# Performance work log

Hardware: AMD Instinct MI355X
Metric: run time of the kernel (lower is better)

Reference implementation:

```python
import jax, jax.numpy as jnp
import numpy as np

B, S, H, NH, NF = 128, 1024, 768, 8, 8
FUSED = 3 * H + NF  # 2312


def _lin(k, o, i):
    return jax.random.normal(k, (o, i), jnp.float32) * (1.0 / np.sqrt(i))


def setup_inputs() -> dict:
    key = jax.random.key(0)
    ks = jax.random.split(key, 20)
    last_hidden = jax.random.normal(ks[0], (B, S, H), jnp.float32)
    arousal_feats = jax.random.normal(ks[1], (B, NF), jnp.float32)
    sep1 = jax.random.randint(ks[2], (B,), 2, 800)
    sep2 = jnp.minimum(sep1 + jax.random.randint(ks[3], (B,), 2, 200), S - 1)
    return {
        "last_hidden": last_hidden,
        "arousal_feats": arousal_feats,
        "sep1": sep1,
        "sep2": sep2,
        "in_proj_w": _lin(ks[4], 3 * H, H),
        "in_proj_b": jnp.zeros((3 * H,), jnp.float32),
        "out_w": _lin(ks[5], H, H),
        "out_b": jnp.zeros((H,), jnp.float32),
        "ln_g": jnp.ones((NF,), jnp.float32),
        "ln_b": jnp.zeros((NF,), jnp.float32),
        "va_w1": _lin(ks[6], 512, FUSED),
        "va_b1": jnp.zeros((512,), jnp.float32),
        "va_w2": _lin(ks[7], 128, 512),
        "va_b2": jnp.zeros((128,), jnp.float32),
        "va_w3": _lin(ks[8], 2, 128),
        "va_b3": jnp.zeros((2,), jnp.float32),
        "pol_w": _lin(ks[9], 3, FUSED),
        "pol_b": jnp.zeros((3,), jnp.float32),
        "aro_w": _lin(ks[10], 3, FUSED),
        "aro_b": jnp.zeros((3,), jnp.float32),
    }


def reference(last_hidden, arousal_feats, sep1, sep2, in_proj_w, in_proj_b,
              out_w, out_b, ln_g, ln_b, va_w1, va_b1, va_w2, va_b2,
              va_w3, va_b3, pol_w, pol_b, aro_w, aro_b):
    b, s, h = last_hidden.shape
    nh, dh = NH, h // NH
    pos = jnp.arange(s)[None, :]  # [1,S]
    # ragged boundaries -> masks (honors s1>1 / s2>s1+1 fallbacks to CLS token)
    text_mask = jnp.where((sep1 > 1)[:, None], (pos >= 1) & (pos < sep1[:, None]), pos == 0)
    asp_mask = jnp.where((sep2 > sep1 + 1)[:, None], (pos > sep1[:, None]) & (pos < sep2[:, None]), pos == 0)
    amf = asp_mask.astype(last_hidden.dtype)
    asp_query = (last_hidden * amf[..., None]).sum(1) / amf.sum(1)[:, None]  # [B,H]
    # MultiheadAttention with a single query per sample, keys/values masked to text span
    wq, wk, wv = jnp.split(in_proj_w, 3, axis=0)
    bq, bk, bv = jnp.split(in_proj_b, 3)
    q = (asp_query @ wq.T + bq).reshape(b, nh, dh)
    k = (last_hidden @ wk.T + bk).reshape(b, s, nh, dh)
    v = (last_hidden @ wv.T + bv).reshape(b, s, nh, dh)
    scale = 1.0 / np.sqrt(dh)
    scores = jnp.einsum('bhd,bshd->bhs', q, k) * scale
    scores = jnp.where(text_mask[:, None, :], scores, -jnp.inf)
    attn = jax.nn.softmax(scores, axis=-1)
    ctx = jnp.einsum('bhs,bshd->bhd', attn, v).reshape(b, h)
    cross = ctx @ out_w.T + out_b  # [B,H]
    # ArousalFeatureNorm ~ LayerNorm over feature dim
    mu = arousal_feats.mean(-1, keepdims=True)
    var = arousal_feats.var(-1, keepdims=True)
    aro_n = (arousal_feats - mu) / jnp.sqrt(var + 1e-5) * ln_g + ln_b
    fused = jnp.concatenate([last_hidden[:, 0], cross, asp_query, aro_n], axis=-1)
    hdn = jax.nn.gelu(fused @ va_w1.T + va_b1, approximate=False)
    hdn = jax.nn.gelu(hdn @ va_w2.T + va_b2, approximate=False)
    va = hdn @ va_w3.T + va_b3
    pol = fused @ pol_w.T + pol_b
    aro = fused @ aro_w.T + aro_b
    return (va, pol, aro)
```

## Files before the change

kernel.cpp:

```cpp
#include <hip/hip_runtime.h>
#include <hip/hip_bf16.h>
#include <math.h>

#define B 128
#define S 1024
#define H 768
#define NH 8
#define DH 96
#define FUSED 2312
#define KCHUNK 128
#define NOUT 544
#define MD 800
#define NZ_NOCTX 13
#define NZ_CTX 5
#define NZTOT 18
#define ASL 8
#define NSL 8
#define FCH 16
#define SCALE 0.10206207261596575f
#define GELU_C 0.70710678118654752f

#define MTILES (17 * 25)
#define HTILES (NZ_NOCTX * 4 * 17)

__device__ __forceinline__ float dot4(float4 a, float4 b) {
    return a.x * b.x + a.y * b.y + a.z * b.z + a.w * b.w;
}
__device__ __forceinline__ float gelu(float x) {
    return 0.5f * x * (1.0f + erff(x * GELU_C));
}

__device__ __forceinline__ const float* wrow_sel(int n, const float* va_w1,
                                                 const float* pol_w,
                                                 const float* aro_w,
                                                 bool& valid) {
    valid = true;
    if (n < 512) return va_w1 + (size_t)n * FUSED;
    if (n < 515) return pol_w + (size_t)(n - 512) * FUSED;
    if (n < 518) return aro_w + (size_t)(n - 515) * FUSED;
    valid = false;
    return va_w1;
}

__global__ __launch_bounds__(256) void k1_aspq_m(
        const float* __restrict__ lh,
        const int* __restrict__ sep1,
        const int* __restrict__ sep2,
        const float* __restrict__ va_w1,
        const float* __restrict__ pol_w,
        const float* __restrict__ aro_w,
        const float* __restrict__ out_w,
        const float* __restrict__ out_b,
        float* __restrict__ aspp,
        float* __restrict__ Mbuf) {
    int bid = blockIdx.x, t = threadIdx.x;
    if (bid < B * ASL) {
        if (t >= 192) return;
        int b = bid >> 3, z = bid & 7;
        int s1 = sep1[b], s2 = sep2[b];
        int lo, hi;
        if (s2 > s1 + 1) { lo = s1 + 1; hi = s2; } else { lo = 0; hi = 1; }
        const float* base = lh + ((size_t)b * S) * H + 4 * t;
        float4 a = {0.f, 0.f, 0.f, 0.f};
        for (int s = lo + z; s < hi; s += ASL) {
            float4 r = *(const float4*)(base + (size_t)s * H);
            a.x += r.x; a.y += r.y; a.z += r.z; a.w += r.w;
        }
        *(float4*)(aspp + (size_t)z * (B * H) + b * H + 4 * t) = a;
        return;
    }
    int j = bid - B * ASL;
    int n0 = (j / 25) * 32, d0 = (j % 25) * 32;
    __shared__ float As[32][33];
    __shared__ float Ws[32][33];
    int tx = t & 31, ty = t >> 5;
    int lr = t >> 3, lc = (t & 7) * 4;
    float acc[4] = {0.f, 0.f, 0.f, 0.f};
    for (int k0 = 0; k0 < H; k0 += 32) {
        {
            int n = n0 + lr;
            bool valid;
            const float* wr = wrow_sel(n, va_w1, pol_w, aro_w, valid);
            float4 a = {0.f, 0.f, 0.f, 0.f};
            if (valid) a = *(const float4*)(wr + H + k0 + lc);
            As[lr][lc] = a.x; As[lr][lc + 1] = a.y;
            As[lr][lc + 2] = a.z; As[lr][lc + 3] = a.w;
        }
        {
            int c = k0 + lr;
            float4 w;
            if (d0 < H) {
                w = *(const float4*)(out_w + (size_t)c * H + d0 + lc);
            } else {
                w.x = (lc == 0) ? out_b[c] : 0.f;
                w.y = 0.f; w.z = 0.f; w.w = 0.f;
            }
            Ws[lc][lr] = w.x; Ws[lc + 1][lr] = w.y;
            Ws[lc + 2][lr] = w.z; Ws[lc + 3][lr] = w.w;
        }
        __syncthreads();
#pragma unroll
        for (int kk = 0; kk < 32; ++kk) {
            float wv = Ws[tx][kk];
#pragma unroll
            for (int i = 0; i < 4; ++i)
                acc[i] += As[ty + 8 * i][kk] * wv;
        }
        __syncthreads();
    }
#pragma unroll
    for (int i = 0; i < 4; ++i)
        Mbuf[(size_t)(n0 + ty + 8 * i) * MD + d0 + tx] = acc[i];
}

__global__ void qu_kernel(const float* __restrict__ aspp,
                          const int* __restrict__ sep1,
                          const int* __restrict__ sep2,
                          const float* __restrict__ wq,
                          const float* __restrict__ bq,
                          const float* __restrict__ wk,
                          float* __restrict__ aspq,
                          float* __restrict__ U) {
    int b = blockIdx.x, h = blockIdx.y, t = threadIdx.x;
    int s1 = sep1[b], s2 = sep2[b];
    int lo, hi;
    if (s2 > s1 + 1) { lo = s1 + 1; hi = s2; } else { lo = 0; hi = 1; }
    float inv = 1.0f / (float)(hi - lo);
    __shared__ float aq[H];
    __shared__ float qh[DH];
    for (int c = t; c < H; c += 256) {
        float a = 0.f;
#pragma unroll
        for (int z = 0; z < ASL; ++z)
            a += aspp[(size_t)z * (B * H) + b * H + c];
        a *= inv;
        aq[c] = a;
        if (h == 0) aspq[b * H + c] = a;
    }
    __syncthreads();
    int wave = t >> 6, lane = t & 63;
#pragma unroll
    for (int i = 0; i < 24; ++i) {
        int d = wave * 24 + i;
        const float* wrow = wq + (size_t)(h * DH + d) * H;
        float a = 0.f;
#pragma unroll
        for (int j = 0; j < H / 64; ++j) a += wrow[lane + 64 * j] * aq[lane + 64 * j];
        for (int off = 32; off; off >>= 1) a += __shfl_xor(a, off);
        if (lane == 0) qh[d] = a + bq[h * DH + d];
    }
    __syncthreads();
    float u0 = 0.f, u1 = 0.f, u2 = 0.f;
    for (int d = 0; d < DH; ++d) {
        const float* wrow = wk + (size_t)(h * DH + d) * H;
        float qd = qh[d];
        u0 += qd * wrow[t];
        u1 += qd * wrow[t + 256];
        u2 += qd * wrow[t + 512];
    }
    float* Ub = U + ((size_t)b * NH + h) * H;
    Ub[t] = u0; Ub[t + 256] = u1; Ub[t + 512] = u2;
}

__global__ __launch_bounds__(512) void k3_flash_hdn1(
        const float* __restrict__ lhg,
        const float* __restrict__ U,
        const int* __restrict__ sep1,
        const float* __restrict__ aspq,
        const float* __restrict__ aro_f,
        const float* __restrict__ ln_g,
        const float* __restrict__ ln_b,
        const float* __restrict__ va_w1,
        const float* __restrict__ pol_w,
        const float* __restrict__ aro_w,
        float* __restrict__ Op,
        float* __restrict__ mlb,
        float* __restrict__ hdn1p) {
    __shared__ float smem[FCH * H];
    int bid = blockIdx.x, t = threadIdx.x;

    if (bid < B * NSL) {
        int b = bid >> 3, z = bid & 7;
        int wave = t >> 6, lane = t & 63;
        int s1 = sep1[b];
        int tlo = (s1 > 1) ? 1 : 0;
        int thi = (s1 > 1) ? s1 : 1;
        int span = thi - tlo;
        int nrows = (span > z) ? ((span - z - 1) / NSL + 1) : 0;
        float (*lhs)[H] = (float(*)[H])smem;

        const float4* Uh = (const float4*)(U + ((size_t)b * NH + wave) * H);
        float4 u0 = Uh[lane], u1 = Uh[lane + 64], u2 = Uh[lane + 128];
        float4 O0 = {0.f, 0.f, 0.f, 0.f}, O1 = O0, O2 = O0;
        float m = -1e30f, l = 0.f;
        int rid = t >> 5, cid = t & 31;

        for (int j0 = 0; j0 < nrows; j0 += FCH) {
            int nv = min(FCH, nrows - j0);
            if (rid < nv) {
                int sg = tlo + z + NSL * (j0 + rid);
                const float4* row = (const float4*)(lhg + ((size_t)b * S + sg) * H);
                float4* dst = (float4*)lhs[rid];
#pragma unroll
                for (int k = 0; k < 6; ++k) dst[cid + 32 * k] = row[cid + 32 * k];
            }
            __syncthreads();
            for (int r = 0; r < nv; ++r) {
                const float4* xr = (const float4*)lhs[r];
                float4 x0 = xr[lane], x1 = xr[lane + 64], x2 = xr[lane + 128];
                float s = dot4(u0, x0) + dot4(u1, x1) + dot4(u2, x2);
                for (int off = 32; off; off >>= 1) s += __shfl_xor(s, off);
                s *= SCALE;
                if (s <= m) {
                    float p = __expf(s - m);
                    l += p;
                    O0.x += p * x0.x; O0.y += p * x0.y; O0.z += p * x0.z; O0.w += p * x0.w;
                    O1.x += p * x1.x; O1.y += p * x1.y; O1.z += p * x1.z; O1.w += p * x1.w;
                    O2.x += p * x2.x; O2.y += p * x2.y; O2.z += p * x2.z; O2.w += p * x2.w;
                } else {
                    float c = __expf(m - s);
                    m = s;
                    l = l * c + 1.0f;
                    O0.x = O0.x * c + x0.x; O0.y = O0.y * c + x0.y;
                    O0.z = O0.z * c + x0.z; O0.w = O0.w * c + x0.w;
                    O1.x = O1.x * c + x1.x; O1.y = O1.y * c + x1.y;
                    O1.z = O1.z * c + x1.z; O1.w = O1.w * c + x1.w;
                    O2.x = O2.x * c + x2.x; O2.y = O2.y * c + x2.y;
                    O2.z = O2.z * c + x2.z; O2.w = O2.w * c + x2.w;
                }
            }
            __syncthreads();
        }
        float4* Ob = (float4*)(Op + (((size_t)z * B + b) * NH + wave) * H);
        Ob[lane] = O0; Ob[lane + 64] = O1; Ob[lane + 128] = O2;
        if (lane == 0) {
            float* ml = mlb + ((size_t)z * B + b) * NH * 2;
            ml[2 * wave]     = m;
            ml[2 * wave + 1] = l;
        }
        return;
    }

    int j = bid - B * NSL;
    int z13 = j / 68, rem = j % 68;
    int z = (z13 < 6) ? z13 : z13 + 6;
    int m0 = (rem / 17) * 32, n0 = (rem % 17) * 32;
    int kbase = z * KCHUNK;
    float (*As)[33] = (float(*)[33])smem;
    float (*Ws)[33] = (float(*)[33])(smem + 32 * 33);
    int tx = t & 31, ty = t >> 5;
    int lr = t >> 3, lc = (t & 7) * 4;
    float acc[4] = {0.f, 0.f, 0.f, 0.f};
    bool active = (t < 256);
    for (int k0 = kbase; k0 < kbase + KCHUNK; k0 += 32) {
        if (active) {
            int bb = m0 + lr;
            int k = k0 + lc;
            float4 a;
            if (k < 768) {
                a = *(const float4*)(lhg + (size_t)bb * S * H + k);
            } else if (k < 2304) {
                a = *(const float4*)(aspq + (size_t)bb * H + (k - 1536));
            } else if (k < FUSED) {
                const float* af = aro_f + bb * 8;
                float mu = 0.f;
#pragma unroll
                for (int jj = 0; jj < 8; ++jj) mu += af[jj];
                mu *= 0.125f;
                float var = 0.f;
#pragma unroll
                for (int jj = 0; jj < 8; ++jj) { float d = af[jj] - mu; var += d * d; }
                var *= 0.125f;
                float rs = rsqrtf(var + 1e-5f);
                int c = k - 2304;
                a.x = (af[c]     - mu) * rs * ln_g[c]     + ln_b[c];
                a.y = (af[c + 1] - mu) * rs * ln_g[c + 1] + ln_b[c + 1];
                a.z = (af[c + 2] - mu) * rs * ln_g[c + 2] + ln_b[c + 2];
                a.w = (af[c + 3] - mu) * rs * ln_g[c + 3] + ln_b[c + 3];
            } else {
                a = {0.f, 0.f, 0.f, 0.f};
            }
            As[lr][lc] = a.x; As[lr][lc + 1] = a.y;
            As[lr][lc + 2] = a.z; As[lr][lc + 3] = a.w;
            int n = n0 + lr;
            int kk = min(k0 + lc, FUSED - 4);
            bool valid;
            const float* wr = wrow_sel(n, va_w1, pol_w, aro_w, valid);
            float4 w = {0.f, 0.f, 0.f, 0.f};
            if (valid) w = *(const float4*)(wr + kk);
            Ws[lr][lc] = w.x; Ws[lr][lc + 1] = w.y;
            Ws[lr][lc + 2] = w.z; Ws[lr][lc + 3] = w.w;
        }
        __syncthreads();
        if (active) {
#pragma unroll
            for (int kk = 0; kk < 32; ++kk) {
                float wv = Ws[tx][kk];
#pragma unroll
                for (int i = 0; i < 4; ++i)
                    acc[i] += As[ty + 8 * i][kk] * wv;
            }
        }
        __syncthreads();
    }
    if (active) {
        int n = n0 + tx;
#pragma unroll
        for (int i = 0; i < 4; ++i) {
            int mm = m0 + ty + 8 * i;
            hdn1p[(size_t)z13 * (B * NOUT) + (size_t)mm * NOUT + n] = acc[i];
        }
    }
}

__global__ void mergectx_kernel(const float* __restrict__ Op,
                                const float* __restrict__ mlb,
                                const float* __restrict__ wv,
                                const float* __restrict__ bv,
                                float* __restrict__ ctx) {
    int b = blockIdx.x, h = blockIdx.y, t = threadIdx.x;
    float M = -1e30f;
#pragma unroll
    for (int z = 0; z < NSL; ++z)
        M = fmaxf(M, mlb[(((size_t)z * B + b) * NH + h) * 2]);
    float wz[NSL], L = 0.f;
#pragma unroll
    for (int z = 0; z < NSL; ++z) {
        const float* ml = mlb + (((size_t)z * B + b) * NH + h) * 2;
        float e = __expf(ml[0] - M);
        wz[z] = e;
        L += e * ml[1];
    }
    float Li = 1.0f / L;
    __shared__ float wsum[H];
    for (int c = t; c < H; c += 256) {
        float a = 0.f;
#pragma unroll
        for (int z = 0; z < NSL; ++z)
            a += wz[z] * Op[(((size_t)z * B + b) * NH + h) * H + c];
        wsum[c] = a * Li;
    }
    __syncthreads();
    int wave = t >> 6, lane = t & 63;
#pragma unroll
    for (int i = 0; i < 24; ++i) {
        int d = wave * 24 + i;
        const float* wrow = wv + (size_t)(h * DH + d) * H;
        float a = 0.f;
#pragma unroll
        for (int j = 0; j < H / 64; ++j) a += wrow[lane + 64 * j] * wsum[lane + 64 * j];
        for (int off = 32; off; off >>= 1) a += __shfl_xor(a, off);
        if (lane == 0) ctx[b * H + h * DH + d] = a + bv[h * DH + d];
    }
}

__global__ __launch_bounds__(256) void k5_hdn1ctx(
        const float* __restrict__ ctx,
        const float* __restrict__ Mbuf,
        float* __restrict__ hdn1p) {
    int z = blockIdx.z;
    int n0 = blockIdx.x * 32, m0 = blockIdx.y * 32;
    int kbase = z * 160;
    __shared__ float As[32][33];
    __shared__ float Ws[32][33];
    int t = threadIdx.x;
    int tx = t & 31, ty = t >> 5;
    int lr = t >> 3, lc = (t & 7) * 4;
    float acc[4] = {0.f, 0.f, 0.f, 0.f};
    for (int k0 = kbase; k0 < kbase + 160; k0 += 32) {
        {
            int bb = m0 + lr;
            int k = k0 + lc;
            float4 a;
            if (k < 768)      a = *(const float4*)(ctx + (size_t)bb * H + k);
            else if (k == 768) a = {1.f, 0.f, 0.f, 0.f};
            else              a = {0.f, 0.f, 0.f, 0.f};
            As[lr][lc] = a.x; As[lr][lc + 1] = a.y;
            As[lr][lc + 2] = a.z; As[lr][lc + 3] = a.w;
        }
        {
            float4 w = *(const float4*)(Mbuf + (size_t)(n0 + lr) * MD + k0 + lc);
            Ws[lr][lc] = w.x; Ws[lr][lc + 1] = w.y;
            Ws[lr][lc + 2] = w.z; Ws[lr][lc + 3] = w.w;
        }
        __syncthreads();
#pragma unroll
        for (int kk = 0; kk < 32; ++kk) {
            float wv = Ws[tx][kk];
#pragma unroll
            for (int i = 0; i < 4; ++i)
                acc[i] += As[ty + 8 * i][kk] * wv;
        }
        __syncthreads();
    }
    int n = n0 + tx;
#pragma unroll
    for (int i = 0; i < 4; ++i) {
        int mm = m0 + ty + 8 * i;
        hdn1p[(size_t)(NZ_NOCTX + z) * (B * NOUT) + (size_t)mm * NOUT + n] = acc[i];
    }
}

__global__ __launch_bounds__(512) void mlp2_kernel(
        const float* __restrict__ hdn1p,
        const float* __restrict__ va_b1,
        const float* __restrict__ va_w2,
        const float* __restrict__ va_b2,
        const float* __restrict__ va_w3,
        const float* __restrict__ va_b3,
        const float* __restrict__ pol_b,
        const float* __restrict__ aro_b,
        float* __restrict__ out) {
    int b = blockIdx.x, t = threadIdx.x;
    int wave = t >> 6, lane = t & 63;
    __shared__ float hsS[512];
    __shared__ float h2S[128];
    {
        float s = 0.f;
#pragma unroll
        for (int z = 0; z < NZTOT; ++z)
            s += hdn1p[(size_t)z * (B * NOUT) + (size_t)b * NOUT + t];
        hsS[t] = gelu(s + va_b1[t]);
    }
    if (t < 6) {
        float s = 0.f;
#pragma unroll
        for (int z = 0; z < NZTOT; ++z)
            s += hdn1p[(size_t)z * (B * NOUT) + (size_t)b * NOUT + 512 + t];
        if (t < 3) out[256 + b * 3 + t]       = s + pol_b[t];
        else       out[640 + b * 3 + (t - 3)] = s + aro_b[t - 3];
    }
    __syncthreads();
#pragma unroll
    for (int i = 0; i < 16; ++i) {
        int n = wave * 16 + i;
        float a = 0.f;
#pragma unroll
        for (int j = 0; j < 8; ++j) {
            int k = lane + 64 * j;
            a += hsS[k] * va_w2[(size_t)n * 512 + k];
        }
        for (int off = 32; off; off >>= 1) a += __shfl_xor(a, off);
        if (lane == 0) h2S[n] = gelu(a + va_b2[n]);
    }
    __syncthreads();
    if (wave < 2) {
        float a = h2S[lane] * va_w3[wave * 128 + lane]
                + h2S[lane + 64] * va_w3[wave * 128 + lane + 64];
        for (int off = 32; off; off >>= 1) a += __shfl_xor(a, off);
        if (lane == 0) out[b * 2 + wave] = a + va_b3[wave];
    }
}

extern "C" void kernel_launch(void* const* d_in, const int* in_sizes, int n_in,
                              void* d_out, int out_size, void* d_ws, size_t ws_size,
                              hipStream_t stream) {
    const float* lh    = (const float*)d_in[0];
    const float* aro_f = (const float*)d_in[1];
    const int*   sep1  = (const int*)d_in[2];
    const int*   sep2  = (const int*)d_in[3];
    const float* in_w  = (const float*)d_in[4];
    const float* in_b  = (const float*)d_in[5];
    const float* out_w = (const float*)d_in[6];
    const float* out_b = (const float*)d_in[7];
    const float* ln_g  = (const float*)d_in[8];
    const float* ln_b  = (const float*)d_in[9];
    const float* va_w1 = (const float*)d_in[10];
    const float* va_b1 = (const float*)d_in[11];
    const float* va_w2 = (const float*)d_in[12];
    const float* va_b2 = (const float*)d_in[13];
    const float* va_w3 = (const float*)d_in[14];
    const float* va_b3 = (const float*)d_in[15];
    const float* pol_w = (const float*)d_in[16];
    const float* pol_b = (const float*)d_in[17];
    const float* aro_w = (const float*)d_in[18];
    const float* aro_b = (const float*)d_in[19];
    float* out = (float*)d_out;

    float* ws = (float*)d_ws;
    float* aspp   = ws;
    float* aspq   = aspp + ASL * B * H;
    float* Ubuf   = aspq + B * H;
    float* Opb    = Ubuf + B * NH * H;
    float* mlbuf  = Opb + (size_t)NSL * B * NH * H;
    float* ctx    = mlbuf + NSL * B * NH * 2;
    float* Mbuf   = ctx + B * H;
    float* hdn1p  = Mbuf + NOUT * MD;

    const float* wq = in_w;
    const float* wk = in_w + H * H;
    const float* wv = in_w + 2 * H * H;
    const float* bq = in_b;
    const float* bv = in_b + 2 * H;

    k1_aspq_m<<<B * ASL + MTILES, 256, 0, stream>>>(
        lh, sep1, sep2, va_w1, pol_w, aro_w, out_w, out_b, aspp, Mbuf);
    qu_kernel<<<dim3(B, NH), 256, 0, stream>>>(aspp, sep1, sep2, wq, bq, wk,
                                               aspq, Ubuf);
    k3_flash_hdn1<<<B * NSL + HTILES, 512, 0, stream>>>(
        lh, Ubuf, sep1, aspq, aro_f, ln_g, ln_b,
        va_w1, pol_w, aro_w, Opb, mlbuf, hdn1p);
    mergectx_kernel<<<dim3(B, NH), 256, 0, stream>>>(Opb, mlbuf, wv, bv, ctx);
    k5_hdn1ctx<<<dim3(17, 4, NZ_CTX), 256, 0, stream>>>(ctx, Mbuf, hdn1p);
    mlp2_kernel<<<B, 512, 0, stream>>>(hdn1p, va_b1, va_w2, va_b2,
                                       va_w3, va_b3, pol_b, aro_b, out);
}
```

Before: 216.0 us.

## Fold ctx projection into mergectx, batch qu over samples, move CLS/aro partials to k1

Drops the separate k5 GEMM by storing a transposed precomputed out_w·va_w1 product and letting mergectx multiply each head's context directly into per-head hidden-layer partial slots. The CLS-token and normalized arousal-feature partial GEMM tiles move from k3 into k1, so k3 only handles the aspect-query K chunks. qu_kernel now handles four samples per block so each wq/wk row is reused across them. This removes one launch and cuts repeated weight reads, at the cost of more partial-sum slots (21) for mlp2 to reduce and a serial per-head dot in mergectx.

```diff
diff --git a/kernel.cpp b/kernel.cpp
--- a/kernel.cpp
+++ b/kernel.cpp
@@ -10,18 +10,18 @@
 #define FUSED 2312
 #define KCHUNK 128
 #define NOUT 544
-#define MD 800
-#define NZ_NOCTX 13
-#define NZ_CTX 5
-#define NZTOT 18
+#define NZTOT 21
 #define ASL 8
 #define NSL 8
 #define FCH 16
+#define NBQ 4
 #define SCALE 0.10206207261596575f
 #define GELU_C 0.70710678118654752f
 
-#define MTILES (17 * 25)
-#define HTILES (NZ_NOCTX * 4 * 17)
+#define AJOBS (B * ASL)
+#define MJOBS (17 * 25)
+#define H1JOBS (7 * 4 * 17)
+#define H3JOBS (6 * 4 * 17)
 
 __device__ __forceinline__ float dot4(float4 a, float4 b) {
     return a.x * b.x + a.y * b.y + a.z * b.z + a.w * b.w;
@@ -42,7 +42,7 @@
     return va_w1;
 }
 
-__global__ __launch_bounds__(256) void k1_aspq_m(
+__global__ __launch_bounds__(256) void k1_kernel(
         const float* __restrict__ lh,
         const int* __restrict__ sep1,
         const int* __restrict__ sep2,
@@ -51,10 +51,14 @@
         const float* __restrict__ aro_w,
         const float* __restrict__ out_w,
         const float* __restrict__ out_b,
+        const float* __restrict__ aro_f,
+        const float* __restrict__ ln_g,
+        const float* __restrict__ ln_b,
         float* __restrict__ aspp,
-        float* __restrict__ Mbuf) {
+        float* __restrict__ MbufT,
+        float* __restrict__ hdn1p) {
     int bid = blockIdx.x, t = threadIdx.x;
-    if (bid < B * ASL) {
+    if (bid < AJOBS) {
         if (t >= 192) return;
         int b = bid >> 3, z = bid & 7;
         int s1 = sep1[b], s2 = sep2[b];
@@ -69,34 +73,94 @@
         *(float4*)(aspp + (size_t)z * (B * H) + b * H + 4 * t) = a;
         return;
     }
-    int j = bid - B * ASL;
-    int n0 = (j / 25) * 32, d0 = (j % 25) * 32;
     __shared__ float As[32][33];
     __shared__ float Ws[32][33];
     int tx = t & 31, ty = t >> 5;
     int lr = t >> 3, lc = (t & 7) * 4;
     float acc[4] = {0.f, 0.f, 0.f, 0.f};
-    for (int k0 = 0; k0 < H; k0 += 32) {
+
+    if (bid < AJOBS + MJOBS) {
+        int j = bid - AJOBS;
+        int n0 = (j / 25) * 32, d0 = (j % 25) * 32;
+        for (int k0 = 0; k0 < H; k0 += 32) {
+            if (d0 < H) {
+                float4 w = *(const float4*)(out_w + (size_t)(k0 + lr) * H + d0 + lc);
+                As[lc][lr] = w.x; As[lc + 1][lr] = w.y;
+                As[lc + 2][lr] = w.z; As[lc + 3][lr] = w.w;
+            } else {
+                float ob = out_b[k0 + lr];
+                As[lc][lr]     = (lc == 0) ? ob : 0.f;
+                As[lc + 1][lr] = 0.f; As[lc + 2][lr] = 0.f; As[lc + 3][lr] = 0.f;
+            }
+            {
+                int n = n0 + lr;
+                bool valid;
+                const float* wr = wrow_sel(n, va_w1, pol_w, aro_w, valid);
+                float4 w = {0.f, 0.f, 0.f, 0.f};
+                if (valid) w = *(const float4*)(wr + H + k0 + lc);
+                Ws[lc][lr] = w.x; Ws[lc + 1][lr] = w.y;
+                Ws[lc + 2][lr] = w.z; Ws[lc + 3][lr] = w.w;
+            }
+            __syncthreads();
+#pragma unroll
+            for (int kk = 0; kk < 32; ++kk) {
+                float wv = Ws[kk][tx];
+#pragma unroll
+                for (int i = 0; i < 4; ++i)
+                    acc[i] += As[ty + 8 * i][kk] * wv;
+            }
+            __syncthreads();
+        }
+#pragma unroll
+        for (int i = 0; i < 4; ++i)
+            MbufT[(size_t)(d0 + ty + 8 * i) * NOUT + n0 + tx] = acc[i];
+        return;
+    }
+
+    int j = bid - AJOBS - MJOBS;
+    int zi = j / 68, rem = j % 68;
+    int z    = (zi < 6) ? zi : 18;
+    int slot = (zi < 6) ? zi : 12;
+    int m0 = (rem / 17) * 32, n0 = (rem % 17) * 32;
+    int kbase = z * KCHUNK;
+    for (int k0 = kbase; k0 < kbase + KCHUNK; k0 += 32) {
+        {
+            int bb = m0 + lr;
+            int k = k0 + lc;
+            float4 a;
+            if (k < 768) {
+                a = *(const float4*)(lh + (size_t)bb * S * H + k);
+            } else if (k < FUSED) {
+                const float* af = aro_f + bb * 8;
+                float mu = 0.f;
+#pragma unroll
+                for (int jj = 0; jj < 8; ++jj) mu += af[jj];
+                mu *= 0.125f;
+                float var = 0.f;
+#pragma unroll
+                for (int jj = 0; jj < 8; ++jj) { float d = af[jj] - mu; var += d * d; }
+                var *= 0.125f;
+                float rs = rsqrtf(var + 1e-5f);
+                int c = k - 2304;
+                a.x = (af[c]     - mu) * rs * ln_g[c]     + ln_b[c];
+                a.y = (af[c + 1] - mu) * rs * ln_g[c + 1] + ln_b[c + 1];
+                a.z = (af[c + 2] - mu) * rs * ln_g[c + 2] + ln_b[c + 2];
+                a.w = (af[c + 3] - mu) * rs * ln_g[c + 3] + ln_b[c + 3];
+            } else {
+                a = {0.f, 0.f, 0.f, 0.f};
+            }
+            As[lr][lc] = a.x; As[lr][lc + 1] = a.y;
+            As[lr][lc + 2] = a.z; As[lr][lc + 3] = a.w;
+        }
         {
             int n = n0 + lr;
+            int kk = min(k0 + lc, FUSED - 4);
             bool valid;
             const float* wr = wrow_sel(n, va_w1, pol_w, aro_w, valid);
-            float4 a = {0.f, 0.f, 0.f, 0.f};
-            if (valid) a = *(const float4*)(wr + H + k0 + lc);
-            As[lr][lc] = a.x; As[lr][lc + 1] = a.y;
-            As[lr][lc + 2] = a.z; As[lr][lc + 3] = a.w;
-        }
-        {
-            int c = k0 + lr;
-            float4 w;
-            if (d0 < H) {
-                w = *(const float4*)(out_w + (size_t)c * H + d0 + lc);
-            } else {
-                w.x = (lc == 0) ? out_b[c] : 0.f;
-                w.y = 0.f; w.z = 0.f; w.w = 0.f;
-            }
-            Ws[lc][lr] = w.x; Ws[lc + 1][lr] = w.y;
-            Ws[lc + 2][lr] = w.z; Ws[lc + 3][lr] = w.w;
+            float4 w = {0.f, 0.f, 0.f, 0.f};
+            if (valid) w = *(const float4*)(wr + kk);
+            Ws[lr][lc] = w.x; Ws[lr][lc + 1] = w.y;
+            Ws[lr][lc + 2] = w.z; Ws[lr][lc + 3] = w.w;
         }
         __syncthreads();
 #pragma unroll
@@ -108,68 +172,102 @@
         }
         __syncthreads();
     }
-#pragma unroll
-    for (int i = 0; i < 4; ++i)
-        Mbuf[(size_t)(n0 + ty + 8 * i) * MD + d0 + tx] = acc[i];
-}
-
-__global__ void qu_kernel(const float* __restrict__ aspp,
-                          const int* __restrict__ sep1,
-                          const int* __restrict__ sep2,
-                          const float* __restrict__ wq,
-                          const float* __restrict__ bq,
-                          const float* __restrict__ wk,
-                          float* __restrict__ aspq,
-                          float* __restrict__ U) {
-    int b = blockIdx.x, h = blockIdx.y, t = threadIdx.x;
-    int s1 = sep1[b], s2 = sep2[b];
-    int lo, hi;
-    if (s2 > s1 + 1) { lo = s1 + 1; hi = s2; } else { lo = 0; hi = 1; }
-    float inv = 1.0f / (float)(hi - lo);
-    __shared__ float aq[H];
-    __shared__ float qh[DH];
-    for (int c = t; c < H; c += 256) {
+    int n = n0 + tx;
+#pragma unroll
+    for (int i = 0; i < 4; ++i) {
+        int mm = m0 + ty + 8 * i;
+        hdn1p[(size_t)slot * (B * NOUT) + (size_t)mm * NOUT + n] = acc[i];
+    }
+}
+
+__global__ __launch_bounds__(512) void qu_kernel(
+        const float* __restrict__ aspp,
+        const int* __restrict__ sep1,
+        const int* __restrict__ sep2,
+        const float* __restrict__ wq,
+        const float* __restrict__ bq,
+        const float* __restrict__ wk,
+        float* __restrict__ aspq,
+        float* __restrict__ U) {
+    int g = blockIdx.x, h = blockIdx.y, t = threadIdx.x;
+    int wave = t >> 6, lane = t & 63;
+    __shared__ float aqS[NBQ][772];
+    __shared__ float qhS[NBQ][DH];
+
+    for (int i = t; i < NBQ * H; i += 512) {
+        int b = i & 3, c = i >> 2;
+        int gb = g * NBQ + b;
+        int s1 = sep1[gb], s2 = sep2[gb];
+        float inv = 1.0f / (float)((s2 > s1 + 1) ? (s2 - s1 - 1) : 1);
         float a = 0.f;
 #pragma unroll
         for (int z = 0; z < ASL; ++z)
-            a += aspp[(size_t)z * (B * H) + b * H + c];
+            a += aspp[(size_t)z * (B * H) + (size_t)gb * H + c];
         a *= inv;
-        aq[c] = a;
-        if (h == 0) aspq[b * H + c] = a;
+        aqS[b][c] = a;
+        if (h == 0) aspq[(size_t)gb * H + c] = a;
     }
     __syncthreads();
-    int wave = t >> 6, lane = t & 63;
-#pragma unroll
-    for (int i = 0; i < 24; ++i) {
-        int d = wave * 24 + i;
-        const float* wrow = wq + (size_t)(h * DH + d) * H;
-        float a = 0.f;
-#pragma unroll
-        for (int j = 0; j < H / 64; ++j) a += wrow[lane + 64 * j] * aq[lane + 64 * j];
-        for (int off = 32; off; off >>= 1) a += __shfl_xor(a, off);
-        if (lane == 0) qh[d] = a + bq[h * DH + d];
+
+    const float4* a40 = (const float4*)aqS[0];
+    const float4* a41 = (const float4*)aqS[1];
+    const float4* a42 = (const float4*)aqS[2];
+    const float4* a43 = (const float4*)aqS[3];
+#pragma unroll
+    for (int dd = 0; dd < 12; ++dd) {
+        int d = wave * 12 + dd;
+        const float4* wr = (const float4*)(wq + (size_t)(h * DH + d) * H);
+        float4 w0 = wr[lane], w1 = wr[lane + 64], w2 = wr[lane + 128];
+        float c0 = dot4(w0, a40[lane]) + dot4(w1, a40[lane + 64]) + dot4(w2, a40[lane + 128]);
+        float c1 = dot4(w0, a41[lane]) + dot4(w1, a41[lane + 64]) + dot4(w2, a41[lane + 128]);
+        float c2 = dot4(w0, a42[lane]) + dot4(w1, a42[lane + 64]) + dot4(w2, a42[lane + 128]);
+        float c3 = dot4(w0, a43[lane]) + dot4(w1, a43[lane + 64]) + dot4(w2, a43[lane + 128]);
+        for (int off = 32; off; off >>= 1) {
+            c0 += __shfl_xor(c0, off);
+            c1 += __shfl_xor(c1, off);
+            c2 += __shfl_xor(c2, off);
+            c3 += __shfl_xor(c3, off);
+        }
+        if (lane == 0) {
+            float bqa = bq[h * DH + d];
+            qhS[0][d] = c0 + bqa; qhS[1][d] = c1 + bqa;
+            qhS[2][d] = c2 + bqa; qhS[3][d] = c3 + bqa;
+        }
     }
     __syncthreads();
-    float u0 = 0.f, u1 = 0.f, u2 = 0.f;
+
+    int c1 = t, c2 = 512 + t;
+    float u00 = 0.f, u10 = 0.f, u20 = 0.f, u30 = 0.f;
+    float u01 = 0.f, u11 = 0.f, u21 = 0.f, u31 = 0.f;
+    bool do2 = (t < 256);
     for (int d = 0; d < DH; ++d) {
+        float q0 = qhS[0][d], q1 = qhS[1][d], q2 = qhS[2][d], q3 = qhS[3][d];
         const float* wrow = wk + (size_t)(h * DH + d) * H;
-        float qd = qh[d];
-        u0 += qd * wrow[t];
-        u1 += qd * wrow[t + 256];
-        u2 += qd * wrow[t + 512];
-    }
-    float* Ub = U + ((size_t)b * NH + h) * H;
-    Ub[t] = u0; Ub[t + 256] = u1; Ub[t + 512] = u2;
-}
-
-__global__ __launch_bounds__(512) void k3_flash_hdn1(
+        float wv1 = wrow[c1];
+        u00 += q0 * wv1; u10 += q1 * wv1; u20 += q2 * wv1; u30 += q3 * wv1;
+        if (do2) {
+            float wv2 = wrow[c2];
+            u01 += q0 * wv2; u11 += q1 * wv2; u21 += q2 * wv2; u31 += q3 * wv2;
+        }
+    }
+    size_t ub = ((size_t)(g * NBQ) * NH + h) * H;
+    U[ub + c1]              = u00;
+    U[ub + NH * H + c1]     = u10;
+    U[ub + 2 * NH * H + c1] = u20;
+    U[ub + 3 * NH * H + c1] = u30;
+    if (do2) {
+        U[ub + c2]              = u01;
+        U[ub + NH * H + c2]     = u11;
+        U[ub + 2 * NH * H + c2] = u21;
+        U[ub + 3 * NH * H + c2] = u31;
+    }
+}
+
+__global__ __launch_bounds__(512) void k3_kernel(
         const float* __restrict__ lhg,
         const float* __restrict__ U,
         const int* __restrict__ sep1,
         const float* __restrict__ aspq,
-        const float* __restrict__ aro_f,
-        const float* __restrict__ ln_g,
-        const float* __restrict__ ln_b,
         const float* __restrict__ va_w1,
         const float* __restrict__ pol_w,
         const float* __restrict__ aro_w,
@@ -242,8 +340,8 @@
     }
 
     int j = bid - B * NSL;
-    int z13 = j / 68, rem = j % 68;
-    int z = (z13 < 6) ? z13 : z13 + 6;
+    int zi = j / 68, rem = j % 68;
+    int z = zi + 12, slot = zi + 6;
     int m0 = (rem / 17) * 32, n0 = (rem % 17) * 32;
     int kbase = z * KCHUNK;
     float (*As)[33] = (float(*)[33])smem;
@@ -256,38 +354,14 @@
         if (active) {
             int bb = m0 + lr;
             int k = k0 + lc;
-            float4 a;
-            if (k < 768) {
-                a = *(const float4*)(lhg + (size_t)bb * S * H + k);
-            } else if (k < 2304) {
-                a = *(const float4*)(aspq + (size_t)bb * H + (k - 1536));
-            } else if (k < FUSED) {
-                const float* af = aro_f + bb * 8;
-                float mu = 0.f;
-#pragma unroll
-                for (int jj = 0; jj < 8; ++jj) mu += af[jj];
-                mu *= 0.125f;
-                float var = 0.f;
-#pragma unroll
-                for (int jj = 0; jj < 8; ++jj) { float d = af[jj] - mu; var += d * d; }
-                var *= 0.125f;
-                float rs = rsqrtf(var + 1e-5f);
-                int c = k - 2304;
-                a.x = (af[c]     - mu) * rs * ln_g[c]     + ln_b[c];
-                a.y = (af[c + 1] - mu) * rs * ln_g[c + 1] + ln_b[c + 1];
-                a.z = (af[c + 2] - mu) * rs * ln_g[c + 2] + ln_b[c + 2];
-                a.w = (af[c + 3] - mu) * rs * ln_g[c + 3] + ln_b[c + 3];
-            } else {
-                a = {0.f, 0.f, 0.f, 0.f};
-            }
+            float4 a = *(const float4*)(aspq + (size_t)bb * H + (k - 1536));
             As[lr][lc] = a.x; As[lr][lc + 1] = a.y;
             As[lr][lc + 2] = a.z; As[lr][lc + 3] = a.w;
             int n = n0 + lr;
-            int kk = min(k0 + lc, FUSED - 4);
             bool valid;
             const float* wr = wrow_sel(n, va_w1, pol_w, aro_w, valid);
             float4 w = {0.f, 0.f, 0.f, 0.f};
-            if (valid) w = *(const float4*)(wr + kk);
+            if (valid) w = *(const float4*)(wr + k);
             Ws[lr][lc] = w.x; Ws[lr][lc + 1] = w.y;
             Ws[lr][lc + 2] = w.z; Ws[lr][lc + 3] = w.w;
         }
@@ -308,17 +382,21 @@
 #pragma unroll
         for (int i = 0; i < 4; ++i) {
             int mm = m0 + ty + 8 * i;
-            hdn1p[(size_t)z13 * (B * NOUT) + (size_t)mm * NOUT + n] = acc[i];
-        }
-    }
-}
-
-__global__ void mergectx_kernel(const float* __restrict__ Op,
-                                const float* __restrict__ mlb,
-                                const float* __restrict__ wv,
-                                const float* __restrict__ bv,
-                                float* __restrict__ ctx) {
+            hdn1p[(size_t)slot * (B * NOUT) + (size_t)mm * NOUT + n] = acc[i];
+        }
+    }
+}
+
+__global__ __launch_bounds__(256) void mergectx_kernel(
+        const float* __restrict__ Op,
+        const float* __restrict__ mlb,
+        const float* __restrict__ wv,
+        const float* __restrict__ bv,
+        const float* __restrict__ MbufT,
+        float* __restrict__ hdn1p) {
     int b = blockIdx.x, h = blockIdx.y, t = threadIdx.x;
+    __shared__ float wsum[H];
+    __shared__ float ctxS[DH];
     float M = -1e30f;
 #pragma unroll
     for (int z = 0; z < NSL; ++z)
@@ -332,7 +410,6 @@
         L += e * ml[1];
     }
     float Li = 1.0f / L;
-    __shared__ float wsum[H];
     for (int c = t; c < H; c += 256) {
         float a = 0.f;
 #pragma unroll
@@ -350,55 +427,26 @@
 #pragma unroll
         for (int j = 0; j < H / 64; ++j) a += wrow[lane + 64 * j] * wsum[lane + 64 * j];
         for (int off = 32; off; off >>= 1) a += __shfl_xor(a, off);
-        if (lane == 0) ctx[b * H + h * DH + d] = a + bv[h * DH + d];
-    }
-}
-
-__global__ __launch_bounds__(256) void k5_hdn1ctx(
-        const float* __restrict__ ctx,
-        const float* __restrict__ Mbuf,
-        float* __restrict__ hdn1p) {
-    int z = blockIdx.z;
-    int n0 = blockIdx.x * 32, m0 = blockIdx.y * 32;
-    int kbase = z * 160;
-    __shared__ float As[32][33];
-    __shared__ float Ws[32][33];
-    int t = threadIdx.x;
-    int tx = t & 31, ty = t >> 5;
-    int lr = t >> 3, lc = (t & 7) * 4;
-    float acc[4] = {0.f, 0.f, 0.f, 0.f};
-    for (int k0 = kbase; k0 < kbase + 160; k0 += 32) {
-        {
-            int bb = m0 + lr;
-            int k = k0 + lc;
-            float4 a;
-            if (k < 768)      a = *(const float4*)(ctx + (size_t)bb * H + k);
-            else if (k == 768) a = {1.f, 0.f, 0.f, 0.f};
-            else              a = {0.f, 0.f, 0.f, 0.f};
-            As[lr][lc] = a.x; As[lr][lc + 1] = a.y;
-            As[lr][lc + 2] = a.z; As[lr][lc + 3] = a.w;
-        }
-        {
-            float4 w = *(const float4*)(Mbuf + (size_t)(n0 + lr) * MD + k0 + lc);
-            Ws[lr][lc] = w.x; Ws[lr][lc + 1] = w.y;
-            Ws[lr][lc + 2] = w.z; Ws[lr][lc + 3] = w.w;
-        }
-        __syncthreads();
-#pragma unroll
-        for (int kk = 0; kk < 32; ++kk) {
-            float wv = Ws[tx][kk];
-#pragma unroll
-            for (int i = 0; i < 4; ++i)
-                acc[i] += As[ty + 8 * i][kk] * wv;
-        }
-        __syncthreads();
-    }
-    int n = n0 + tx;
-#pragma unroll
-    for (int i = 0; i < 4; ++i) {
-        int mm = m0 + ty + 8 * i;
-        hdn1p[(size_t)(NZ_NOCTX + z) * (B * NOUT) + (size_t)mm * NOUT + n] = acc[i];
-    }
+        if (lane == 0) ctxS[d] = a + bv[h * DH + d];
+    }
+    __syncthreads();
+    int n0 = t, n1 = t + 256, n2 = (t < 32) ? t + 512 : 543;
+    float a0 = 0.f, a1 = 0.f, a2 = 0.f;
+    for (int d = 0; d < DH; ++d) {
+        float cv = ctxS[d];
+        const float* Mr = MbufT + (size_t)(h * DH + d) * NOUT;
+        a0 += Mr[n0] * cv;
+        a1 += Mr[n1] * cv;
+        a2 += Mr[n2] * cv;
+    }
+    if (h == 0) {
+        const float* Mb = MbufT + (size_t)768 * NOUT;
+        a0 += Mb[n0]; a1 += Mb[n1]; a2 += Mb[n2];
+    }
+    float* hp = hdn1p + (size_t)(13 + h) * (B * NOUT) + (size_t)b * NOUT;
+    hp[n0] = a0;
+    hp[n1] = a1;
+    if (t < 32) hp[n2] = a2;
 }
 
 __global__ __launch_bounds__(512) void mlp2_kernel(
@@ -483,25 +531,23 @@
     float* Ubuf   = aspq + B * H;
     float* Opb    = Ubuf + B * NH * H;
     float* mlbuf  = Opb + (size_t)NSL * B * NH * H;
-    float* ctx    = mlbuf + NSL * B * NH * 2;
-    float* Mbuf   = ctx + B * H;
-    float* hdn1p  = Mbuf + NOUT * MD;
+    float* MbufT  = mlbuf + NSL * B * NH * 2;
+    float* hdn1p  = MbufT + 800 * NOUT;
 
     const float* wq = in_w;
     const float* wk = in_w + H * H;
     const float* wv = in_w + 2 * H * H;
     const float* bq = in_b;
-    const float* bv = in_b + 2 * H;
-
-    k1_aspq_m<<<B * ASL + MTILES, 256, 0, stream>>>(
-        lh, sep1, sep2, va_w1, pol_w, aro_w, out_w, out_b, aspp, Mbuf);
-    qu_kernel<<<dim3(B, NH), 256, 0, stream>>>(aspp, sep1, sep2, wq, bq, wk,
-                                               aspq, Ubuf);
-    k3_flash_hdn1<<<B * NSL + HTILES, 512, 0, stream>>>(
-        lh, Ubuf, sep1, aspq, aro_f, ln_g, ln_b,
-        va_w1, pol_w, aro_w, Opb, mlbuf, hdn1p);
-    mergectx_kernel<<<dim3(B, NH), 256, 0, stream>>>(Opb, mlbuf, wv, bv, ctx);
-    k5_hdn1ctx<<<dim3(17, 4, NZ_CTX), 256, 0, stream>>>(ctx, Mbuf, hdn1p);
+
+    k1_kernel<<<AJOBS + MJOBS + H1JOBS, 256, 0, stream>>>(
+        lh, sep1, sep2, va_w1, pol_w, aro_w, out_w, out_b,
+        aro_f, ln_g, ln_b, aspp, MbufT, hdn1p);
+    qu_kernel<<<dim3(B / NBQ, NH), 512, 0, stream>>>(
+        aspp, sep1, sep2, wq, bq, wk, aspq, Ubuf);
+    k3_kernel<<<B * NSL + H3JOBS, 512, 0, stream>>>(
+        lh, Ubuf, sep1, aspq, va_w1, pol_w, aro_w, Opb, mlbuf, hdn1p);
+    mergectx_kernel<<<dim3(B, NH), 256, 0, stream>>>(
+        Opb, mlbuf, wv, in_b + 2 * H, MbufT, hdn1p);
     mlp2_kernel<<<B, 512, 0, stream>>>(hdn1p, va_b1, va_w2, va_b2,
                                        va_w3, va_b3, pol_b, aro_b, out);
 }
```

Result: slower. 288.1 us (+33.4%).
